# Kernel optimization log

Hardware: AMD Instinct MI355X
Metric: run time of the kernel (lower is better)

Reference implementation:

```python
import jax, jax.numpy as jnp
import numpy as np

B, T, D = 64, 4096, 512


def setup_inputs() -> dict:
    key = jax.random.key(0)
    k1, k2, k3, k4 = jax.random.split(key, 4)
    query = jax.random.normal(k1, (B, D), dtype=jnp.float32)
    attend_to = jax.random.normal(k2, (B, T, D), dtype=jnp.float32)
    mask = jax.random.randint(k3, (T, B), 0, 2).astype(bool)  # True = masked out
    # xavier_normal_ for Linear(D, D): std = sqrt(2/(D+D))
    W = jax.random.normal(k4, (D, D), dtype=jnp.float32) * np.sqrt(2.0 / (D + D)).astype(np.float32)
    b = jnp.zeros((D,), dtype=jnp.float32)
    return {"query": query, "attend_to": attend_to, "mask": mask, "W": W, "b": b}


def reference(query, attend_to, mask, W, b):
    # key = Linear(query): [B, D]
    k = query @ W.T + b
    # align[t, b] = attend_to[b, t, :] . k[b, :]  (computed as [B, T] directly)
    scores = jnp.einsum("btd,bd->bt", attend_to, k)
    # masked_fill_(mask.bool(), -inf); mask is [T, B] -> transpose to [B, T]
    scores = jnp.where(mask.T, -jnp.inf, scores)
    # softmax over T (original: transpose to [B, T] then softmax dim=1)
    align = jax.nn.softmax(scores, axis=1)  # [B, T]
    # context = align.unsqueeze(1).bmm(attended.transpose(1,0)) -> [B, 1, D]
    context = jnp.einsum("bt,btd->bd", align, attend_to)[:, None, :]
    return context
```

## Files before the change

kernel.cpp:

```cpp
#include <hip/hip_runtime.h>
#include <math.h>

#define B_ 64
#define T_ 4096
#define D_ 512
#define S_ 32
#define TS_ (T_ / S_)
#define WPT_ (TS_ / 4)

__global__ __launch_bounds__(256) void key_kernel(const float* __restrict__ query,
                                                  const float* __restrict__ W,
                                                  const float* __restrict__ bias,
                                                  float* __restrict__ k) {
    const int b = blockIdx.y;
    const int d = blockIdx.x * 256 + threadIdx.x;
    __shared__ float4 q[D_ / 4];
    const float4* qrow = (const float4*)(query + (size_t)b * D_);
    if (threadIdx.x < D_ / 4) q[threadIdx.x] = qrow[threadIdx.x];
    __syncthreads();
    const float4* Wd = (const float4*)(W + (size_t)d * D_);
    float acc = bias[d];
#pragma unroll 8
    for (int j = 0; j < D_ / 4; ++j) {
        float4 w4 = Wd[j];
        float4 q4 = q[j];
        acc += q4.x * w4.x + q4.y * w4.y + q4.z * w4.z + q4.w * w4.w;
    }
    k[(size_t)b * D_ + d] = acc;
}

__global__ __launch_bounds__(256) void attn_partial_kernel(const float* __restrict__ attend_to,
                                                           const int* __restrict__ mask,
                                                           const float* __restrict__ k,
                                                           float* __restrict__ part_acc,
                                                           float* __restrict__ part_m,
                                                           float* __restrict__ part_l) {
    const int s    = blockIdx.x;
    const int b    = blockIdx.y;
    const int tid  = threadIdx.x;
    const int w    = tid >> 6;
    const int lane = tid & 63;

    const float4* krow = (const float4*)(k + (size_t)b * D_);
    const float4 k0 = krow[lane];
    const float4 k1 = krow[64 + lane];

    float m = -INFINITY;
    float l = 0.0f;
    float4 a0 = make_float4(0.f, 0.f, 0.f, 0.f);
    float4 a1 = make_float4(0.f, 0.f, 0.f, 0.f);

    const int t_base = s * TS_ + w * WPT_;
    for (int i = 0; i < WPT_; ++i) {
        const int t = t_base + i;
        if (mask[t * B_ + b]) continue;
        const float4* vrow = (const float4*)(attend_to + ((size_t)b * T_ + t) * D_);
        const float4 v0 = vrow[lane];
        const float4 v1 = vrow[64 + lane];
        float p = v0.x * k0.x + v0.y * k0.y + v0.z * k0.z + v0.w * k0.w
                + v1.x * k1.x + v1.y * k1.y + v1.z * k1.z + v1.w * k1.w;
#pragma unroll
        for (int off = 32; off > 0; off >>= 1) p += __shfl_xor(p, off, 64);

        if (p > m) {
            const float alpha = __expf(m - p);
            l *= alpha;
            a0.x *= alpha; a0.y *= alpha; a0.z *= alpha; a0.w *= alpha;
            a1.x *= alpha; a1.y *= alpha; a1.z *= alpha; a1.w *= alpha;
            m = p;
        }
        const float e = __expf(p - m);
        l += e;
        a0.x += e * v0.x; a0.y += e * v0.y; a0.z += e * v0.z; a0.w += e * v0.w;
        a1.x += e * v1.x; a1.y += e * v1.y; a1.z += e * v1.z; a1.w += e * v1.w;
    }

    __shared__ float red_acc[4][D_];
    __shared__ float red_m[4];
    __shared__ float red_l[4];
    ((float4*)red_acc[w])[lane]      = a0;
    ((float4*)red_acc[w])[64 + lane] = a1;
    if (lane == 0) { red_m[w] = m; red_l[w] = l; }
    __syncthreads();

    const float m0 = red_m[0], m1 = red_m[1], m2 = red_m[2], m3 = red_m[3];
    const float mb = fmaxf(fmaxf(m0, m1), fmaxf(m2, m3));
    const float s0 = (red_l[0] == 0.f) ? 0.f : __expf(m0 - mb);
    const float s1 = (red_l[1] == 0.f) ? 0.f : __expf(m1 - mb);
    const float s2 = (red_l[2] == 0.f) ? 0.f : __expf(m2 - mb);
    const float s3 = (red_l[3] == 0.f) ? 0.f : __expf(m3 - mb);
    const float lb = red_l[0] * s0 + red_l[1] * s1 + red_l[2] * s2 + red_l[3] * s3;

    const int ps = b * S_ + s;
    float* pa = part_acc + (size_t)ps * D_;
#pragma unroll
    for (int d = tid; d < D_; d += 256) {
        pa[d] = red_acc[0][d] * s0 + red_acc[1][d] * s1 + red_acc[2][d] * s2 + red_acc[3][d] * s3;
    }
    if (tid == 0) { part_m[ps] = mb; part_l[ps] = lb; }
}

__global__ __launch_bounds__(256) void attn_final_kernel(const float* __restrict__ part_acc,
                                                         const float* __restrict__ part_m,
                                                         const float* __restrict__ part_l,
                                                         float* __restrict__ out) {
    const int b = blockIdx.x;
    const int tid = threadIdx.x;
    __shared__ float sc[S_];

    float mstar = -INFINITY;
#pragma unroll
    for (int s = 0; s < S_; ++s) mstar = fmaxf(mstar, part_m[b * S_ + s]);
    if (tid < S_) {
        const float ls = part_l[b * S_ + tid];
        sc[tid] = (ls == 0.f) ? 0.f : __expf(part_m[b * S_ + tid] - mstar);
    }
    __syncthreads();

    float ltot = 0.f;
#pragma unroll
    for (int s = 0; s < S_; ++s) ltot += part_l[b * S_ + s] * sc[s];
    const float inv = 1.0f / ltot;

#pragma unroll
    for (int d = tid; d < D_; d += 256) {
        float acc = 0.f;
#pragma unroll
        for (int s = 0; s < S_; ++s)
            acc += part_acc[((size_t)(b * S_ + s)) * D_ + d] * sc[s];
        out[(size_t)b * D_ + d] = acc * inv;
    }
}

extern "C" void kernel_launch(void* const* d_in, const int* in_sizes, int n_in,
                              void* d_out, int out_size, void* d_ws, size_t ws_size,
                              hipStream_t stream) {
    const float* query     = (const float*)d_in[0];
    const float* attend_to = (const float*)d_in[1];
    const int*   mask      = (const int*)d_in[2];
    const float* W         = (const float*)d_in[3];
    const float* bias      = (const float*)d_in[4];
    float* out = (float*)d_out;

    float* ws       = (float*)d_ws;
    float* k        = ws;
    float* part_acc = k + B_ * D_;
    float* part_m   = part_acc + B_ * S_ * D_;
    float* part_l   = part_m + B_ * S_;

    key_kernel<<<dim3(2, B_), 256, 0, stream>>>(query, W, bias, k);
    attn_partial_kernel<<<dim3(S_, B_), 256, 0, stream>>>(attend_to, mask, k,
                                                          part_acc, part_m, part_l);
    attn_final_kernel<<<dim3(B_), 256, 0, stream>>>(part_acc, part_m, part_l, out);
}
```

Measured before the change: 663.4 us.

## Ballot mask upfront and process four unmasked rows per iteration

Each wave now loads its 32 mask entries in one ballot, then walks the active bits, handling four unmasked rows per iteration with batched loads, interleaved shuffle reductions and one shared max update. This removes the serial per-row mask load and branch, and raises memory-level parallelism so more row loads are in flight per wave. The cost is higher register pressure from holding four row vectors, and padded duplicate loads when fewer than four rows remain.

```diff
diff --git a/kernel.cpp b/kernel.cpp
--- a/kernel.cpp
+++ b/kernel.cpp
@@ -45,34 +45,77 @@
     const float4 k0 = krow[lane];
     const float4 k1 = krow[64 + lane];
 
+    const int t_base = s * TS_ + w * WPT_;
+    const int probe_t = t_base + (lane & 31);
+    const bool active_lane = (lane < WPT_) && (mask[probe_t * B_ + b] == 0);
+    unsigned long long act = __ballot(active_lane);
+
     float m = -INFINITY;
     float l = 0.0f;
     float4 a0 = make_float4(0.f, 0.f, 0.f, 0.f);
     float4 a1 = make_float4(0.f, 0.f, 0.f, 0.f);
 
-    const int t_base = s * TS_ + w * WPT_;
-    for (int i = 0; i < WPT_; ++i) {
-        const int t = t_base + i;
-        if (mask[t * B_ + b]) continue;
-        const float4* vrow = (const float4*)(attend_to + ((size_t)b * T_ + t) * D_);
-        const float4 v0 = vrow[lane];
-        const float4 v1 = vrow[64 + lane];
-        float p = v0.x * k0.x + v0.y * k0.y + v0.z * k0.z + v0.w * k0.w
-                + v1.x * k1.x + v1.y * k1.y + v1.z * k1.z + v1.w * k1.w;
+    const float* rowbase = attend_to + ((size_t)b * T_ + t_base) * D_;
+
+    while (act) {
+        int i0 = __ffsll(act) - 1; act &= act - 1;
+        bool h1 = (act != 0);
+        int i1 = h1 ? (__ffsll(act) - 1) : i0; act &= act - 1;
+        bool h2 = (act != 0);
+        int i2 = h2 ? (__ffsll(act) - 1) : i0; act &= act - 1;
+        bool h3 = (act != 0);
+        int i3 = h3 ? (__ffsll(act) - 1) : i0; act &= act - 1;
+
+        const float4* r0 = (const float4*)(rowbase + (size_t)i0 * D_);
+        const float4* r1 = (const float4*)(rowbase + (size_t)i1 * D_);
+        const float4* r2 = (const float4*)(rowbase + (size_t)i2 * D_);
+        const float4* r3 = (const float4*)(rowbase + (size_t)i3 * D_);
+        const float4 v00 = r0[lane], v01 = r0[64 + lane];
+        const float4 v10 = r1[lane], v11 = r1[64 + lane];
+        const float4 v20 = r2[lane], v21 = r2[64 + lane];
+        const float4 v30 = r3[lane], v31 = r3[64 + lane];
+
+        float p0 = v00.x * k0.x + v00.y * k0.y + v00.z * k0.z + v00.w * k0.w
+                 + v01.x * k1.x + v01.y * k1.y + v01.z * k1.z + v01.w * k1.w;
+        float p1 = v10.x * k0.x + v10.y * k0.y + v10.z * k0.z + v10.w * k0.w
+                 + v11.x * k1.x + v11.y * k1.y + v11.z * k1.z + v11.w * k1.w;
+        float p2 = v20.x * k0.x + v20.y * k0.y + v20.z * k0.z + v20.w * k0.w
+                 + v21.x * k1.x + v21.y * k1.y + v21.z * k1.z + v21.w * k1.w;
+        float p3 = v30.x * k0.x + v30.y * k0.y + v30.z * k0.z + v30.w * k0.w
+                 + v31.x * k1.x + v31.y * k1.y + v31.z * k1.z + v31.w * k1.w;
+
 #pragma unroll
-        for (int off = 32; off > 0; off >>= 1) p += __shfl_xor(p, off, 64);
+        for (int off = 32; off > 0; off >>= 1) {
+            p0 += __shfl_xor(p0, off, 64);
+            p1 += __shfl_xor(p1, off, 64);
+            p2 += __shfl_xor(p2, off, 64);
+            p3 += __shfl_xor(p3, off, 64);
+        }
+        if (!h1) p1 = -INFINITY;
+        if (!h2) p2 = -INFINITY;
+        if (!h3) p3 = -INFINITY;
 
-        if (p > m) {
-            const float alpha = __expf(m - p);
+        const float mb = fmaxf(fmaxf(p0, p1), fmaxf(p2, p3));
+        if (mb > m) {
+            const float alpha = __expf(m - mb);
             l *= alpha;
             a0.x *= alpha; a0.y *= alpha; a0.z *= alpha; a0.w *= alpha;
             a1.x *= alpha; a1.y *= alpha; a1.z *= alpha; a1.w *= alpha;
-            m = p;
+            m = mb;
         }
-        const float e = __expf(p - m);
-        l += e;
-        a0.x += e * v0.x; a0.y += e * v0.y; a0.z += e * v0.z; a0.w += e * v0.w;
-        a1.x += e * v1.x; a1.y += e * v1.y; a1.z += e * v1.z; a1.w += e * v1.w;
+        const float e0 = __expf(p0 - m);
+        const float e1 = __expf(p1 - m);
+        const float e2 = __expf(p2 - m);
+        const float e3 = __expf(p3 - m);
+        l += e0 + e1 + e2 + e3;
+        a0.x += e0 * v00.x + e1 * v10.x + e2 * v20.x + e3 * v30.x;
+        a0.y += e0 * v00.y + e1 * v10.y + e2 * v20.y + e3 * v30.y;
+        a0.z += e0 * v00.z + e1 * v10.z + e2 * v20.z + e3 * v30.z;
+        a0.w += e0 * v00.w + e1 * v10.w + e2 * v20.w + e3 * v30.w;
+        a1.x += e0 * v01.x + e1 * v11.x + e2 * v21.x + e3 * v31.x;
+        a1.y += e0 * v01.y + e1 * v11.y + e2 * v21.y + e3 * v31.y;
+        a1.z += e0 * v01.z + e1 * v11.z + e2 * v21.z + e3 * v31.z;
+        a1.w += e0 * v01.w + e1 * v11.w + e2 * v21.w + e3 * v31.w;
     }
 
     __shared__ float red_acc[4][D_];
```

New measurement: 661.9 us. About the same (-0.2%).
